# Optimization experiments

Hardware: AMD Instinct MI355X
Metric: run time of the kernel (lower is better)

Reference implementation:

```python
import jax, jax.numpy as jnp
import numpy as np

B, H, W, C = 4, 64, 64, 256
C8 = C // 8

def setup_inputs() -> dict:
    key = jax.random.key(0)
    k1, k2, k3, k4 = jax.random.split(key, 4)
    # glorot-uniform-ish init for 1x1 conv kernels stored as [Cin, Cout]
    def glorot(k, cin, cout):
        lim = np.sqrt(6.0 / (cin + cout)).astype(np.float32)
        return jax.random.uniform(k, (cin, cout), jnp.float32, -lim, lim)
    return {
        "x": jax.random.normal(k1, (B, H, W, C), jnp.float32),
        "kernel_f": glorot(k2, C, C8),
        "kernel_g": glorot(k3, C, C8),
        "kernel_h": glorot(k4, C, C),
        "gamma": jnp.zeros((1,), jnp.float32),
    }

def reference(x, kernel_f, kernel_g, kernel_h, gamma):
    b, h, w, c = x.shape
    n = h * w
    xf = x.reshape(b, n, c)                       # [B, N, C]
    # 1x1 convs == per-position matmuls
    f = jnp.einsum('bnc,cd->bnd', xf, kernel_f)   # [B, N, C/8]
    g = jnp.einsum('bnc,cd->bnd', xf, kernel_g)   # [B, N, C/8]
    hh = jnp.einsum('bnc,cd->bnd', xf, kernel_h)  # [B, N, C]
    s = jnp.einsum('bnd,bmd->bnm', g, f)          # [B, N, N]
    beta = jax.nn.softmax(s, axis=-1)
    o = jnp.einsum('bnm,bmc->bnc', beta, hh)      # [B, N, C]
    o = o.reshape(b, h, w, c)
    return gamma * o + x
```

## Files before the change

### kernel.cpp

```cpp
#include <hip/hip_runtime.h>
#include <hip/hip_bf16.h>

typedef __bf16 bf16x8 __attribute__((ext_vector_type(8)));
typedef float f32x4 __attribute__((ext_vector_type(4)));
typedef float f32x16 __attribute__((ext_vector_type(16)));
typedef unsigned short u16;
typedef unsigned int u32;

__device__ __forceinline__ u16 f2bf_rne(float f){
  union { float f; u32 u; } v; v.f = f;
  u32 r = v.u + 0x7fffu + ((v.u >> 16) & 1u);
  return (u16)(r >> 16);
}
__device__ __forceinline__ u32 pack2(float a, float b){
  return __builtin_amdgcn_perm(__float_as_uint(a), __float_as_uint(b), 0x03020706u);
}
#define BARRIER_LGKM() asm volatile("s_waitcnt lgkmcnt(0)\n\ts_barrier" ::: "memory")

__global__ __launch_bounds__(512) void prep_kernel(
    const float* __restrict__ Wf, const float* __restrict__ Wg,
    const float* __restrict__ Wh, u16* __restrict__ Wfrag){
  const int cc = blockIdx.x;
  const int t = threadIdx.x;
  const int kk = t >> 6, lane = t & 63;
  const int L = lane & 15, quad = lane >> 4;
  const int n = cc * 16 + L;
  u32 pk[4];
  #pragma unroll
  for (int j2 = 0; j2 < 4; ++j2){
    float v[2];
    #pragma unroll
    for (int h = 0; h < 2; ++h){
      int k = kk * 32 + quad * 8 + j2 * 2 + h;
      if (n < 256)      v[h] = Wh[k * 256 + n];
      else if (n < 288) v[h] = Wf[k * 32 + (n - 256)];
      else              v[h] = Wg[k * 32 + (n - 288)];
    }
    pk[j2] = (u32)f2bf_rne(v[0]) | ((u32)f2bf_rne(v[1]) << 16);
  }
  uint4* dst = (uint4*)(Wfrag + ((size_t)(cc * 8 + kk) * 64 + lane) * 8);
  *dst = make_uint4(pk[0], pk[1], pk[2], pk[3]);
}

__global__ __launch_bounds__(512) void proj_kernel(
    const float* __restrict__ x, const u16* __restrict__ Wfrag,
    u16* __restrict__ Qg, u16* __restrict__ Kg, u16* __restrict__ Vfrag)
{
  __shared__ __align__(16) u16 smem[256 * 72];
  u16 (*xb)[264] = (u16(*)[264])smem;
  u16 (*Vr)[72]  = (u16(*)[72])smem;

  const int tid = threadIdx.x;
  const int lane = tid & 63, wave = tid >> 6;
  const int L = lane & 15, quad = lane >> 4;
  const int rowgrp = wave >> 1, colhalf = wave & 1;
  const int n0 = blockIdx.x * 64;

  const float4* xsrc = (const float4*)(x + (size_t)n0 * 256);
  #pragma unroll
  for (int j = 0; j < 8; ++j){
    int idx = j * 512 + tid;
    int row = idx >> 6, col4 = idx & 63;
    float4 v = xsrc[idx];
    u32 p0 = (u32)f2bf_rne(v.x) | ((u32)f2bf_rne(v.y) << 16);
    u32 p1 = (u32)f2bf_rne(v.z) | ((u32)f2bf_rne(v.w) << 16);
    *(uint2*)&xb[row][col4 * 4] = make_uint2(p0, p1);
  }
  __syncthreads();

  f32x4 acc[10];
  #pragma unroll
  for (int cc = 0; cc < 10; ++cc) acc[cc] = (f32x4){0.f, 0.f, 0.f, 0.f};

  #pragma unroll
  for (int kk = 0; kk < 8; ++kk){
    bf16x8 a = *(const bf16x8*)&xb[rowgrp * 16 + L][kk * 32 + quad * 8];
    #pragma unroll
    for (int cc = 0; cc < 10; ++cc){
      int ccg = colhalf * 10 + cc;
      bf16x8 bfr = *(const bf16x8*)(Wfrag + ((size_t)(ccg * 8 + kk) * 64 + lane) * 8);
      acc[cc] = __builtin_amdgcn_mfma_f32_16x16x32_bf16(a, bfr, acc[cc], 0, 0, 0);
    }
  }

  if (colhalf){
    #pragma unroll
    for (int cc = 6; cc < 10; ++cc){
      int ccg = 10 + cc;
      u16* dst = (ccg < 18) ? Kg : Qg;
      float sc = (ccg < 18) ? 1.0f : 1.44269504088896f;
      int c = (ccg & 1) * 16 + L;
      #pragma unroll
      for (int r = 0; r < 4; ++r){
        int row = n0 + rowgrp * 16 + quad * 4 + r;
        dst[(size_t)row * 32 + c] = f2bf_rne(acc[cc][r] * sc);
      }
    }
  }

  __syncthreads();

  {
    const int cmax = colhalf ? 6 : 10;
    for (int cc = 0; cc < cmax; ++cc){
      int ccg = colhalf * 10 + cc;
      int c = ccg * 16 + L;
      #pragma unroll
      for (int r = 0; r < 4; ++r){
        int tn = rowgrp * 16 + quad * 4 + r;
        int p  = ((tn & 15) << 2) | (tn >> 4);
        Vr[c][p] = f2bf_rne(acc[cc][r]);
      }
    }
  }
  __syncthreads();

  u16* Vblk = Vfrag + (size_t)blockIdx.x * (256 * 64);
  #pragma unroll
  for (int i = 0; i < 4; ++i){
    int idx = i * 512 + tid;
    *(uint4*)(Vblk + (size_t)idx * 8) = *(const uint4*)&Vr[idx & 255][(idx >> 8) * 8];
  }
}

__global__ __launch_bounds__(512) void flash_kernel(
    const u16* __restrict__ Qg, const u16* __restrict__ Kg, const u16* __restrict__ Vfrag,
    u16* __restrict__ Opart, float* __restrict__ Lpart)
{
  constexpr float SH = -92.33248261689366f;
  __shared__ __align__(16) u16 Plds[2][128][72];

  const int tid = threadIdx.x, lane = tid & 63, wave = tid >> 6;
  const int L = lane & 15, quad = lane >> 4;
  const int m32 = lane & 31, h32 = lane >> 5;
  const int wq = wave >> 2, wc = wave & 3;

  const int id = blockIdx.x;
  const int slot = id >> 3;
  const int combo = (id & 7) * 2 + (slot >> 5);
  const int qblk = (slot & 31) * 128;
  const int b = combo >> 2, split = combo & 3;

  const u16* Qb = Qg + (size_t)(b * 4096) * 32;
  const u16* Kb = Kg + (size_t)(b * 4096) * 32;
  const u16* Vb = Vfrag + (size_t)b * (64 * 256 * 64);

  const int g0 = split * 16;

  bf16x8 qa = *(const bf16x8*)(Qb + (size_t)(qblk + wave * 16 + L) * 32 + quad * 8);
  const u16* kp0 = Kb + (size_t)(g0 * 64 + L) * 32 + quad * 8;
  bf16x8 kc0 = *(const bf16x8*)(kp0);
  bf16x8 kc1 = *(const bf16x8*)(kp0 + 512);
  bf16x8 kc2 = *(const bf16x8*)(kp0 + 1024);
  bf16x8 kc3 = *(const bf16x8*)(kp0 + 1536);

  bf16x8 vfc[8];
  {
    const u16* Vt = Vb + (size_t)g0 * (256 * 64);
    #pragma unroll
    for (int ks = 0; ks < 4; ++ks){
      const u16* vrow = Vt + (size_t)((ks * 2 + h32) * 256 + wc * 64 + m32) * 8;
      vfc[ks * 2]     = *(const bf16x8*)(vrow);
      vfc[ks * 2 + 1] = *(const bf16x8*)(vrow + 32 * 8);
    }
  }

  f32x16 acc[4];
  #pragma unroll
  for (int t = 0; t < 4; ++t)
    #pragma unroll
    for (int i = 0; i < 16; ++i) acc[t][i] = 0.f;
  float lsum[4] = {0.f, 0.f, 0.f, 0.f};
  const f32x4 zero = (f32x4){0.f, 0.f, 0.f, 0.f};

  for (int kt = 0; kt < 16; ++kt){
    const int g = g0 + kt;
    u16 (*Pw)[72] = Plds[kt & 1];

    f32x4 s0 = __builtin_amdgcn_mfma_f32_16x16x32_bf16(qa, kc0, zero, 0, 0, 0);
    f32x4 s1 = __builtin_amdgcn_mfma_f32_16x16x32_bf16(qa, kc1, zero, 0, 0, 0);
    f32x4 s2 = __builtin_amdgcn_mfma_f32_16x16x32_bf16(qa, kc2, zero, 0, 0, 0);
    f32x4 s3 = __builtin_amdgcn_mfma_f32_16x16x32_bf16(qa, kc3, zero, 0, 0, 0);

    if (kt < 15){
      const u16* kpn = Kb + (size_t)((g + 1) * 64 + L) * 32 + quad * 8;
      kc0 = *(const bf16x8*)(kpn);
      kc1 = *(const bf16x8*)(kpn + 512);
      kc2 = *(const bf16x8*)(kpn + 1024);
      kc3 = *(const bf16x8*)(kpn + 1536);
    }

    #pragma unroll
    for (int r = 0; r < 4; ++r){
      float p0 = __builtin_amdgcn_exp2f(s0[r] + SH);
      float p1 = __builtin_amdgcn_exp2f(s1[r] + SH);
      float p2 = __builtin_amdgcn_exp2f(s2[r] + SH);
      float p3 = __builtin_amdgcn_exp2f(s3[r] + SH);
      lsum[r] += (p0 + p1) + (p2 + p3);
      *(uint2*)&Pw[wave * 16 + quad * 4 + r][L * 4] =
          make_uint2(pack2(p0, p1), pack2(p2, p3));
    }

    BARRIER_LGKM();

    #pragma unroll
    for (int ks = 0; ks < 4; ++ks){
      bf16x8 af0 = *(const bf16x8*)&Pw[wq * 64 + m32][ks * 16 + h32 * 8];
      bf16x8 af1 = *(const bf16x8*)&Pw[wq * 64 + 32 + m32][ks * 16 + h32 * 8];
      acc[0] = __builtin_amdgcn_mfma_f32_32x32x16_bf16(af0, vfc[ks*2],   acc[0], 0, 0, 0);
      acc[1] = __builtin_amdgcn_mfma_f32_32x32x16_bf16(af0, vfc[ks*2+1], acc[1], 0, 0, 0);
      acc[2] = __builtin_amdgcn_mfma_f32_32x32x16_bf16(af1, vfc[ks*2],   acc[2], 0, 0, 0);
      acc[3] = __builtin_amdgcn_mfma_f32_32x32x16_bf16(af1, vfc[ks*2+1], acc[3], 0, 0, 0);
    }

    if (kt < 15){
      const u16* Vn = Vb + (size_t)(g + 1) * (256 * 64);
      #pragma unroll
      for (int ks = 0; ks < 4; ++ks){
        const u16* vrow = Vn + (size_t)((ks * 2 + h32) * 256 + wc * 64 + m32) * 8;
        vfc[ks * 2]     = *(const bf16x8*)(vrow);
        vfc[ks * 2 + 1] = *(const bf16x8*)(vrow + 32 * 8);
      }
    }
  }

  u16* Ob = Opart + ((size_t)split * 16384 + (size_t)b * 4096 + qblk) * 256;
  #pragma unroll
  for (int t = 0; t < 4; ++t){
    const int qi = t >> 1, ci = t & 1;
    #pragma unroll
    for (int rg = 0; rg < 16; ++rg){
      int row = wq * 64 + qi * 32 + (rg & 3) + 8 * (rg >> 2) + 4 * h32;
      int c = wc * 64 + ci * 32 + m32;
      Ob[(size_t)row * 256 + c] = (u16)(__float_as_uint(acc[t][rg]) >> 16);
    }
  }
  #pragma unroll
  for (int r = 0; r < 4; ++r){
    lsum[r] += __shfl_xor(lsum[r], 1);
    lsum[r] += __shfl_xor(lsum[r], 2);
    lsum[r] += __shfl_xor(lsum[r], 4);
    lsum[r] += __shfl_xor(lsum[r], 8);
  }
  if (L == 0){
    float* Lp = Lpart + split * 16384 + b * 4096 + qblk + wave * 16;
    #pragma unroll
    for (int r = 0; r < 4; ++r) Lp[quad * 4 + r] = lsum[r];
  }
}

__global__ __launch_bounds__(256) void combine_kernel(
    const float* __restrict__ x, const float* __restrict__ gamma,
    const u16* __restrict__ Opart, const float* __restrict__ Lpart,
    float* __restrict__ out)
{
  const int t = threadIdx.x;
  const int row = blockIdx.x * 8 + (t >> 5);
  const int c0 = (t & 31) * 8;
  const size_t base = (size_t)row * 256 + c0;
  float os[8];
  #pragma unroll
  for (int i = 0; i < 8; ++i) os[i] = 0.f;
  float ls = 0.f;
  #pragma unroll
  for (int s = 0; s < 4; ++s){
    ls += Lpart[s * 16384 + row];
    uint4 u = *(const uint4*)(Opart + (size_t)s * 16384 * 256 + base);
    os[0] += __uint_as_float(u.x << 16);
    os[1] += __uint_as_float(u.x & 0xffff0000u);
    os[2] += __uint_as_float(u.y << 16);
    os[3] += __uint_as_float(u.y & 0xffff0000u);
    os[4] += __uint_as_float(u.z << 16);
    os[5] += __uint_as_float(u.z & 0xffff0000u);
    os[6] += __uint_as_float(u.w << 16);
    os[7] += __uint_as_float(u.w & 0xffff0000u);
  }
  const float r = gamma[0] / ls;
  float4 x0 = *(const float4*)(x + base);
  float4 x1 = *(const float4*)(x + base + 4);
  float4 o0, o1;
  o0.x = os[0] * r + x0.x;  o0.y = os[1] * r + x0.y;
  o0.z = os[2] * r + x0.z;  o0.w = os[3] * r + x0.w;
  o1.x = os[4] * r + x1.x;  o1.y = os[5] * r + x1.y;
  o1.z = os[6] * r + x1.z;  o1.w = os[7] * r + x1.w;
  *(float4*)(out + base)     = o0;
  *(float4*)(out + base + 4) = o1;
}

extern "C" void kernel_launch(void* const* d_in, const int* in_sizes, int n_in,
                              void* d_out, int out_size, void* d_ws, size_t ws_size,
                              hipStream_t stream) {
  const float* x     = (const float*)d_in[0];
  const float* Wf    = (const float*)d_in[1];
  const float* Wg    = (const float*)d_in[2];
  const float* Wh    = (const float*)d_in[3];
  const float* gamma = (const float*)d_in[4];
  float* out = (float*)d_out;

  u16* p = (u16*)d_ws;
  u16* Qg    = p;  p += 16384 * 32;
  u16* Kg    = p;  p += 16384 * 32;
  u16* Vfrag = p;  p += 4 * 64 * 256 * 64;
  u16* Wfrag = p;  p += 20 * 8 * 64 * 8;
  u16* Opart = p;  p += (size_t)4 * 16384 * 256;
  float* Lpart = (float*)p;

  prep_kernel<<<20, 512, 0, stream>>>(Wf, Wg, Wh, Wfrag);
  proj_kernel<<<256, 512, 0, stream>>>(x, Wfrag, Qg, Kg, Vfrag);
  flash_kernel<<<512, 512, 0, stream>>>(Qg, Kg, Vfrag, Opart, Lpart);
  combine_kernel<<<2048, 256, 0, stream>>>(x, gamma, Opart, Lpart, out);
}
```

Before: 157.0 us.

## Fuse split-K combine into flash kernel via intra-block LDS reduction

The flash kernel now handles a 64-query tile per block, with the two wave-halves each covering half of the key range (32 key tiles apiece). The halves' partial outputs and softmax sums are merged in shared memory, and the gamma scale plus residual add are done in the same kernel. This drops the separate combine kernel and the bf16 partial-output round trip through global memory. In exchange it launches half as many blocks, runs a longer serial loop per wave, and uses 64KB of LDS, which may reduce occupancy.

Result: faster. 149.3 us (-4.9%).

```diff
diff --git a/kernel.cpp b/kernel.cpp
--- a/kernel.cpp
+++ b/kernel.cpp
@@ -125,29 +125,33 @@
 
 __global__ __launch_bounds__(512) void flash_kernel(
     const u16* __restrict__ Qg, const u16* __restrict__ Kg, const u16* __restrict__ Vfrag,
-    u16* __restrict__ Opart, float* __restrict__ Lpart)
+    const float* __restrict__ x, const float* __restrict__ gamma, float* __restrict__ out)
 {
   constexpr float SH = -92.33248261689366f;
-  __shared__ __align__(16) u16 Plds[2][128][72];
+  __shared__ __align__(16) char smem[65536];
+  u16 (*Plds)[2][64][72] = (u16 (*)[2][64][72])smem;
+  float (*Osh)[256] = (float (*)[256])smem;
+  __shared__ float Lsh[2][64];
 
   const int tid = threadIdx.x, lane = tid & 63, wave = tid >> 6;
   const int L = lane & 15, quad = lane >> 4;
   const int m32 = lane & 31, h32 = lane >> 5;
-  const int wq = wave >> 2, wc = wave & 3;
+  const int half = wave >> 2, wv = wave & 3;
 
   const int id = blockIdx.x;
-  const int slot = id >> 3;
-  const int combo = (id & 7) * 2 + (slot >> 5);
-  const int qblk = (slot & 31) * 128;
-  const int b = combo >> 2, split = combo & 3;
+  const int xcd = id & 7;
+  const int b = xcd >> 1;
+  const int qt = (xcd & 1) * 32 + (id >> 3);
+  const int q0 = qt * 64;
 
   const u16* Qb = Qg + (size_t)(b * 4096) * 32;
   const u16* Kb = Kg + (size_t)(b * 4096) * 32;
   const u16* Vb = Vfrag + (size_t)b * (64 * 256 * 64);
-
-  const int g0 = split * 16;
-
-  bf16x8 qa = *(const bf16x8*)(Qb + (size_t)(qblk + wave * 16 + L) * 32 + quad * 8);
+  const float gm = gamma[0];
+
+  const int g0 = half * 32;
+
+  bf16x8 qa = *(const bf16x8*)(Qb + (size_t)(q0 + wv * 16 + L) * 32 + quad * 8);
   const u16* kp0 = Kb + (size_t)(g0 * 64 + L) * 32 + quad * 8;
   bf16x8 kc0 = *(const bf16x8*)(kp0);
   bf16x8 kc1 = *(const bf16x8*)(kp0 + 512);
@@ -159,7 +163,7 @@
     const u16* Vt = Vb + (size_t)g0 * (256 * 64);
     #pragma unroll
     for (int ks = 0; ks < 4; ++ks){
-      const u16* vrow = Vt + (size_t)((ks * 2 + h32) * 256 + wc * 64 + m32) * 8;
+      const u16* vrow = Vt + (size_t)((ks * 2 + h32) * 256 + wv * 64 + m32) * 8;
       vfc[ks * 2]     = *(const bf16x8*)(vrow);
       vfc[ks * 2 + 1] = *(const bf16x8*)(vrow + 32 * 8);
     }
@@ -173,16 +177,16 @@
   float lsum[4] = {0.f, 0.f, 0.f, 0.f};
   const f32x4 zero = (f32x4){0.f, 0.f, 0.f, 0.f};
 
-  for (int kt = 0; kt < 16; ++kt){
+  for (int kt = 0; kt < 32; ++kt){
     const int g = g0 + kt;
-    u16 (*Pw)[72] = Plds[kt & 1];
+    u16 (*Pw)[72] = Plds[half][kt & 1];
 
     f32x4 s0 = __builtin_amdgcn_mfma_f32_16x16x32_bf16(qa, kc0, zero, 0, 0, 0);
     f32x4 s1 = __builtin_amdgcn_mfma_f32_16x16x32_bf16(qa, kc1, zero, 0, 0, 0);
     f32x4 s2 = __builtin_amdgcn_mfma_f32_16x16x32_bf16(qa, kc2, zero, 0, 0, 0);
     f32x4 s3 = __builtin_amdgcn_mfma_f32_16x16x32_bf16(qa, kc3, zero, 0, 0, 0);
 
-    if (kt < 15){
+    if (kt < 31){
       const u16* kpn = Kb + (size_t)((g + 1) * 64 + L) * 32 + quad * 8;
       kc0 = *(const bf16x8*)(kpn);
       kc1 = *(const bf16x8*)(kpn + 512);
@@ -197,7 +201,7 @@
       float p2 = __builtin_amdgcn_exp2f(s2[r] + SH);
       float p3 = __builtin_amdgcn_exp2f(s3[r] + SH);
       lsum[r] += (p0 + p1) + (p2 + p3);
-      *(uint2*)&Pw[wave * 16 + quad * 4 + r][L * 4] =
+      *(uint2*)&Pw[wv * 16 + quad * 4 + r][L * 4] =
           make_uint2(pack2(p0, p1), pack2(p2, p3));
     }
 
@@ -205,36 +209,27 @@
 
     #pragma unroll
     for (int ks = 0; ks < 4; ++ks){
-      bf16x8 af0 = *(const bf16x8*)&Pw[wq * 64 + m32][ks * 16 + h32 * 8];
-      bf16x8 af1 = *(const bf16x8*)&Pw[wq * 64 + 32 + m32][ks * 16 + h32 * 8];
+      bf16x8 af0 = *(const bf16x8*)&Pw[m32][ks * 16 + h32 * 8];
+      bf16x8 af1 = *(const bf16x8*)&Pw[32 + m32][ks * 16 + h32 * 8];
       acc[0] = __builtin_amdgcn_mfma_f32_32x32x16_bf16(af0, vfc[ks*2],   acc[0], 0, 0, 0);
       acc[1] = __builtin_amdgcn_mfma_f32_32x32x16_bf16(af0, vfc[ks*2+1], acc[1], 0, 0, 0);
       acc[2] = __builtin_amdgcn_mfma_f32_32x32x16_bf16(af1, vfc[ks*2],   acc[2], 0, 0, 0);
       acc[3] = __builtin_amdgcn_mfma_f32_32x32x16_bf16(af1, vfc[ks*2+1], acc[3], 0, 0, 0);
     }
 
-    if (kt < 15){
+    if (kt < 31){
       const u16* Vn = Vb + (size_t)(g + 1) * (256 * 64);
       #pragma unroll
       for (int ks = 0; ks < 4; ++ks){
-        const u16* vrow = Vn + (size_t)((ks * 2 + h32) * 256 + wc * 64 + m32) * 8;
+        const u16* vrow = Vn + (size_t)((ks * 2 + h32) * 256 + wv * 64 + m32) * 8;
         vfc[ks * 2]     = *(const bf16x8*)(vrow);
         vfc[ks * 2 + 1] = *(const bf16x8*)(vrow + 32 * 8);
       }
     }
   }
 
-  u16* Ob = Opart + ((size_t)split * 16384 + (size_t)b * 4096 + qblk) * 256;
-  #pragma unroll
-  for (int t = 0; t < 4; ++t){
-    const int qi = t >> 1, ci = t & 1;
-    #pragma unroll
-    for (int rg = 0; rg < 16; ++rg){
-      int row = wq * 64 + qi * 32 + (rg & 3) + 8 * (rg >> 2) + 4 * h32;
-      int c = wc * 64 + ci * 32 + m32;
-      Ob[(size_t)row * 256 + c] = (u16)(__float_as_uint(acc[t][rg]) >> 16);
-    }
-  }
+  BARRIER_LGKM();
+
   #pragma unroll
   for (int r = 0; r < 4; ++r){
     lsum[r] += __shfl_xor(lsum[r], 1);
@@ -243,48 +238,50 @@
     lsum[r] += __shfl_xor(lsum[r], 8);
   }
   if (L == 0){
-    float* Lp = Lpart + split * 16384 + b * 4096 + qblk + wave * 16;
-    #pragma unroll
-    for (int r = 0; r < 4; ++r) Lp[quad * 4 + r] = lsum[r];
-  }
-}
-
-__global__ __launch_bounds__(256) void combine_kernel(
-    const float* __restrict__ x, const float* __restrict__ gamma,
-    const u16* __restrict__ Opart, const float* __restrict__ Lpart,
-    float* __restrict__ out)
-{
-  const int t = threadIdx.x;
-  const int row = blockIdx.x * 8 + (t >> 5);
-  const int c0 = (t & 31) * 8;
-  const size_t base = (size_t)row * 256 + c0;
-  float os[8];
-  #pragma unroll
-  for (int i = 0; i < 8; ++i) os[i] = 0.f;
-  float ls = 0.f;
-  #pragma unroll
-  for (int s = 0; s < 4; ++s){
-    ls += Lpart[s * 16384 + row];
-    uint4 u = *(const uint4*)(Opart + (size_t)s * 16384 * 256 + base);
-    os[0] += __uint_as_float(u.x << 16);
-    os[1] += __uint_as_float(u.x & 0xffff0000u);
-    os[2] += __uint_as_float(u.y << 16);
-    os[3] += __uint_as_float(u.y & 0xffff0000u);
-    os[4] += __uint_as_float(u.z << 16);
-    os[5] += __uint_as_float(u.z & 0xffff0000u);
-    os[6] += __uint_as_float(u.w << 16);
-    os[7] += __uint_as_float(u.w & 0xffff0000u);
-  }
-  const float r = gamma[0] / ls;
-  float4 x0 = *(const float4*)(x + base);
-  float4 x1 = *(const float4*)(x + base + 4);
-  float4 o0, o1;
-  o0.x = os[0] * r + x0.x;  o0.y = os[1] * r + x0.y;
-  o0.z = os[2] * r + x0.z;  o0.w = os[3] * r + x0.w;
-  o1.x = os[4] * r + x1.x;  o1.y = os[5] * r + x1.y;
-  o1.z = os[6] * r + x1.z;  o1.w = os[7] * r + x1.w;
-  *(float4*)(out + base)     = o0;
-  *(float4*)(out + base + 4) = o1;
+    #pragma unroll
+    for (int r = 0; r < 4; ++r) Lsh[half][wv * 16 + quad * 4 + r] = lsum[r];
+  }
+  if (half == 1){
+    #pragma unroll
+    for (int t = 0; t < 4; ++t){
+      const int qi = t >> 1, ci = t & 1;
+      #pragma unroll
+      for (int rg = 0; rg < 16; ++rg){
+        int row = qi * 32 + (rg & 3) + 8 * (rg >> 2) + 4 * h32;
+        Osh[row][wv * 64 + ci * 32 + m32] = acc[t][rg];
+      }
+    }
+  }
+  __syncthreads();
+  if (wave == 0){
+    float li = gm / (Lsh[0][lane] + Lsh[1][lane]);
+    Lsh[0][lane] = li;
+  }
+  __syncthreads();
+  if (half == 0){
+    #pragma unroll
+    for (int t = 0; t < 4; ++t){
+      const int qi = t >> 1, ci = t & 1;
+      #pragma unroll
+      for (int rg = 0; rg < 16; ++rg){
+        int row = qi * 32 + (rg & 3) + 8 * (rg >> 2) + 4 * h32;
+        int col = wv * 64 + ci * 32 + m32;
+        Osh[row][col] = (acc[t][rg] + Osh[row][col]) * Lsh[0][row];
+      }
+    }
+  }
+  __syncthreads();
+  const size_t base = ((size_t)(b * 4096) + q0) * 256;
+  const float4* xs = (const float4*)(x + base);
+  float4* od = (float4*)(out + base);
+  const float4* Of = (const float4*)&Osh[0][0];
+  #pragma unroll
+  for (int i = 0; i < 8; ++i){
+    int idx = i * 512 + tid;
+    float4 o = Of[idx], xv = xs[idx];
+    o.x += xv.x; o.y += xv.y; o.z += xv.z; o.w += xv.w;
+    od[idx] = o;
+  }
 }
 
 extern "C" void kernel_launch(void* const* d_in, const int* in_sizes, int n_in,
@@ -302,11 +299,8 @@
   u16* Kg    = p;  p += 16384 * 32;
   u16* Vfrag = p;  p += 4 * 64 * 256 * 64;
   u16* Wfrag = p;  p += 20 * 8 * 64 * 8;
-  u16* Opart = p;  p += (size_t)4 * 16384 * 256;
-  float* Lpart = (float*)p;
 
   prep_kernel<<<20, 512, 0, stream>>>(Wf, Wg, Wh, Wfrag);
   proj_kernel<<<256, 512, 0, stream>>>(x, Wfrag, Qg, Kg, Vfrag);
-  flash_kernel<<<512, 512, 0, stream>>>(Qg, Kg, Vfrag, Opart, Lpart);
-  combine_kernel<<<2048, 256, 0, stream>>>(x, gamma, Opart, Lpart, out);
-}
+  flash_kernel<<<256, 512, 0, stream>>>(Qg, Kg, Vfrag, x, gamma, out);
+}
```
